# Optimization experiments

Hardware: AMD Instinct MI355X
Metric: run time of the kernel (lower is better)

## Reference

```python
import jax, jax.numpy as jnp
import numpy as np

NEG = jnp.float32(-1e10)

def setup_inputs() -> dict:
    key = jax.random.key(0)
    k1, k2, k3, k4 = jax.random.split(key, 4)
    B, Ns, Nr, D = 64, 512, 256, 1024
    return {
        "span_embeddings": jax.random.normal(k1, (B, Ns, D), dtype=jnp.float32),
        "image_embeddings": jax.random.normal(k2, (B, Nr, D), dtype=jnp.float32),
        "span_mask": jax.random.randint(k3, (B, Ns), 0, 2).astype(jnp.int32),
        "image_mask": jax.random.randint(k4, (B, Nr), 0, 2).astype(jnp.int32),
    }

def reference(span_embeddings, image_embeddings, span_mask, image_mask):
    # pair mask: (B, Ns, Nr) = image_mask[b, None, r] * span_mask[b, s, None]
    mask = (image_mask[:, None, :] * span_mask[:, :, None]).astype(span_embeddings.dtype)
    # QK^T with multiplicative mask, then custom zero->-1e10 masking
    att = jnp.einsum('bsd,brd->bsr', span_embeddings, image_embeddings) * mask
    att = jnp.where(att != 0, att, NEG)
    # spans attend over ROIs
    w_first = jax.nn.softmax(att, axis=-1) * mask
    att_first = jnp.einsum('bsr,brd->bsd', w_first, image_embeddings)
    score = jnp.mean(jnp.square(span_embeddings - att_first))
    # ROIs attend over spans (score_type='both')
    att_t = jnp.swapaxes(att, 1, 2)            # (B, Nr, Ns)
    w_second = jax.nn.softmax(att_t, axis=-1) * jnp.swapaxes(mask, 1, 2)
    att_second = jnp.einsum('brs,bsd->brd', w_second, span_embeddings)
    score = score + jnp.mean(jnp.square(image_embeddings - att_second))
    return score, att_first, att
```

## Files before the change

### kernel.cpp

```cpp
#include <hip/hip_runtime.h>
#include <hip/hip_bf16.h>
#include <math.h>

#define B_  64
#define NS  512
#define NR  256
#define DD  1024
#define NEGV (-1e10f)

typedef __attribute__((ext_vector_type(4))) float f32x4;
typedef __attribute__((ext_vector_type(8))) short bf16x8;

__device__ __forceinline__ unsigned short f2bf(float x) {
    unsigned u = __builtin_bit_cast(unsigned, x);
    unsigned r = u + 0x7FFFu + ((u >> 16) & 1u);
    return (unsigned short)(r >> 16);
}
__device__ __forceinline__ unsigned pk2(float x, float y) {
    unsigned r;
    asm("v_cvt_pk_bf16_f32 %0, %1, %2" : "=v"(r) : "v"(x), "v"(y));
    return r;
}
__device__ __forceinline__ void gload16(const void* g, void* l) {
    __builtin_amdgcn_global_load_lds((const __attribute__((address_space(1))) void*)g,
                                     (__attribute__((address_space(3))) void*)l, 16, 0, 0);
}

__global__ __launch_bounds__(64) void zero_ws(double* ws) {
    if (threadIdx.x == 0) { ws[0] = 0.0; ws[1] = 0.0; }
}

__global__ __launch_bounds__(512) void att_mfma(
    const float* __restrict__ span, const float* __restrict__ image,
    const int* __restrict__ smask, const int* __restrict__ imask,
    float* __restrict__ att, float2* __restrict__ rowP, float2* __restrict__ colP,
    int doStats) {
    const int b  = blockIdx.z;
    const int s0 = blockIdx.y * 128;
    const int r0 = blockIdx.x * 128;
    __shared__ unsigned short Abuf[128][40], Bbuf[128][40];
    const int tid  = threadIdx.x;
    const int lane = tid & 63;
    const int w    = tid >> 6;
    const int wso  = (w >> 2) * 64;
    const int wro  = (w & 3) * 32;
    const float* Sp = span  + ((size_t)b * NS + s0) * DD;
    const float* Im = image + ((size_t)b * NR + r0) * DD;

    f32x4 acc[4][2];
    #pragma unroll
    for (int i = 0; i < 4; ++i)
        #pragma unroll
        for (int j = 0; j < 2; ++j) acc[i][j] = (f32x4){0.f, 0.f, 0.f, 0.f};

    const int row0 = tid >> 2;
    const int kq   = (tid & 3) * 8;
    const int fr   = lane & 15;
    const int fq   = lane >> 4;
    const int fk   = fq * 8;

    for (int k0 = 0; k0 < DD; k0 += 32) {
        {
            const float4 a0 = *reinterpret_cast<const float4*>(Sp + (size_t)row0 * DD + k0 + kq);
            const float4 a1 = *reinterpret_cast<const float4*>(Sp + (size_t)row0 * DD + k0 + kq + 4);
            const float4 c0 = *reinterpret_cast<const float4*>(Im + (size_t)row0 * DD + k0 + kq);
            const float4 c1 = *reinterpret_cast<const float4*>(Im + (size_t)row0 * DD + k0 + kq + 4);
            uint4 u;
            u.x = pk2(a0.x, a0.y); u.y = pk2(a0.z, a0.w);
            u.z = pk2(a1.x, a1.y); u.w = pk2(a1.z, a1.w);
            *reinterpret_cast<uint4*>(&Abuf[row0][kq]) = u;
            u.x = pk2(c0.x, c0.y); u.y = pk2(c0.z, c0.w);
            u.z = pk2(c1.x, c1.y); u.w = pk2(c1.z, c1.w);
            *reinterpret_cast<uint4*>(&Bbuf[row0][kq]) = u;
        }
        __syncthreads();
        bf16x8 ah[4], bh[2];
        #pragma unroll
        for (int mf = 0; mf < 4; ++mf)
            ah[mf] = *reinterpret_cast<const bf16x8*>(&Abuf[wso + mf * 16 + fr][fk]);
        #pragma unroll
        for (int nf = 0; nf < 2; ++nf)
            bh[nf] = *reinterpret_cast<const bf16x8*>(&Bbuf[wro + nf * 16 + fr][fk]);
        #pragma unroll
        for (int mf = 0; mf < 4; ++mf)
            #pragma unroll
            for (int nf = 0; nf < 2; ++nf)
                acc[mf][nf] = __builtin_amdgcn_mfma_f32_16x16x32_bf16(ah[mf], bh[nf], acc[mf][nf], 0, 0, 0);
        __syncthreads();
    }

    float2* rowLDS = reinterpret_cast<float2*>(&Abuf[0][0]);
    float2* colLDS = rowLDS + 512;
    int imv[2];
    #pragma unroll
    for (int nf = 0; nf < 2; ++nf) imv[nf] = imask[b * NR + r0 + wro + nf * 16 + fr];
    float cmax[2] = {-3.4e38f, -3.4e38f};
    float smv[4][4];
    #pragma unroll
    for (int mf = 0; mf < 4; ++mf) {
        #pragma unroll
        for (int i = 0; i < 4; ++i) {
            const int s = s0 + wso + mf * 16 + fq * 4 + i;
            const int sm = smask[b * NS + s];
            smv[mf][i] = (float)sm;
            float* orow = att + ((size_t)b * NS + s) * NR + r0 + wro;
            float vj[2];
            #pragma unroll
            for (int nf = 0; nf < 2; ++nf) {
                float v = acc[mf][nf][i] * (float)(sm * imv[nf]);
                v = (v != 0.0f) ? v : NEGV;
                orow[nf * 16 + fr] = v;
                vj[nf] = v;
                cmax[nf] = fmaxf(cmax[nf], v);
            }
            if (doStats) {
                float rm = fmaxf(vj[0], vj[1]);
                rm = fmaxf(rm, __shfl_xor(rm, 1));
                rm = fmaxf(rm, __shfl_xor(rm, 2));
                rm = fmaxf(rm, __shfl_xor(rm, 4));
                rm = fmaxf(rm, __shfl_xor(rm, 8));
                float rs = __expf(vj[0] - rm) + __expf(vj[1] - rm);
                rs += __shfl_xor(rs, 1);
                rs += __shfl_xor(rs, 2);
                rs += __shfl_xor(rs, 4);
                rs += __shfl_xor(rs, 8);
                if (fr == 0) rowLDS[(wso + mf * 16 + fq * 4 + i) * 4 + (w & 3)] = make_float2(rm, rs);
            }
        }
    }
    if (doStats) {
        #pragma unroll
        for (int nf = 0; nf < 2; ++nf) {
            cmax[nf] = fmaxf(cmax[nf], __shfl_xor(cmax[nf], 16));
            cmax[nf] = fmaxf(cmax[nf], __shfl_xor(cmax[nf], 32));
        }
        float csum[2] = {0.f, 0.f};
        #pragma unroll
        for (int mf = 0; mf < 4; ++mf)
            #pragma unroll
            for (int i = 0; i < 4; ++i)
                #pragma unroll
                for (int nf = 0; nf < 2; ++nf) {
                    float v = acc[mf][nf][i] * (smv[mf][i] * (float)imv[nf]);
                    v = (v != 0.0f) ? v : NEGV;
                    csum[nf] += __expf(v - cmax[nf]);
                }
        #pragma unroll
        for (int nf = 0; nf < 2; ++nf) {
            csum[nf] += __shfl_xor(csum[nf], 16);
            csum[nf] += __shfl_xor(csum[nf], 32);
        }
        if (lane < 16) {
            #pragma unroll
            for (int nf = 0; nf < 2; ++nf)
                colLDS[(wro + nf * 16 + lane) * 2 + (w >> 2)] = make_float2(cmax[nf], csum[nf]);
        }
        __syncthreads();
        if (tid < 128) {
            float2 q0 = rowLDS[tid * 4 + 0], q1 = rowLDS[tid * 4 + 1];
            float2 q2 = rowLDS[tid * 4 + 2], q3 = rowLDS[tid * 4 + 3];
            const float m = fmaxf(fmaxf(q0.x, q1.x), fmaxf(q2.x, q3.x));
            const float ssum = q0.y * __expf(q0.x - m) + q1.y * __expf(q1.x - m)
                             + q2.y * __expf(q2.x - m) + q3.y * __expf(q3.x - m);
            rowP[((size_t)b * NS + s0 + tid) * 2 + blockIdx.x] = make_float2(m, ssum);
        } else if (tid < 256) {
            const int c = tid - 128;
            const float2 q0 = colLDS[c * 2 + 0], q1 = colLDS[c * 2 + 1];
            const float m = fmaxf(q0.x, q1.x);
            const float ssum = q0.y * __expf(q0.x - m) + q1.y * __expf(q1.x - m);
            colP[((size_t)b * NR + r0 + c) * 4 + blockIdx.y] = make_float2(m, ssum);
        }
    }
}

__global__ __launch_bounds__(256) void combine_stats(
    const float2* __restrict__ rowP, const float2* __restrict__ colP,
    const int* __restrict__ smask, const int* __restrict__ imask,
    float* __restrict__ m1, float* __restrict__ f1,
    float* __restrict__ m2, float* __restrict__ f2) {
    const int idx = blockIdx.x * 256 + threadIdx.x;
    if (idx < B_ * NS) {
        const float2 p0 = rowP[(size_t)idx * 2 + 0];
        const float2 p1 = rowP[(size_t)idx * 2 + 1];
        const float m = fmaxf(p0.x, p1.x);
        const float s = p0.y * __expf(p0.x - m) + p1.y * __expf(p1.x - m);
        m1[idx] = m;
        f1[idx] = (float)smask[idx] / s;
    } else if (idx < B_ * NS + B_ * NR) {
        const int j = idx - B_ * NS;
        const float2 p0 = colP[(size_t)j * 4 + 0];
        const float2 p1 = colP[(size_t)j * 4 + 1];
        const float2 p2 = colP[(size_t)j * 4 + 2];
        const float2 p3 = colP[(size_t)j * 4 + 3];
        const float m = fmaxf(fmaxf(p0.x, p1.x), fmaxf(p2.x, p3.x));
        const float s = p0.y * __expf(p0.x - m) + p1.y * __expf(p1.x - m)
                      + p2.y * __expf(p2.x - m) + p3.y * __expf(p3.x - m);
        m2[j] = m;
        f2[j] = (float)imask[j] / s;
    }
}

__global__ __launch_bounds__(256) void transpose_swz(
    const float* __restrict__ src, unsigned short* __restrict__ dst, int N) {
    const int b = blockIdx.z, n0 = blockIdx.y * 32, d0 = blockIdx.x * 32;
    __shared__ unsigned short T[32][36];
    const int t = threadIdx.x;
    {
        const int n = t >> 3, dq = (t & 7) * 4;
        const float4 v = *reinterpret_cast<const float4*>(src + ((size_t)b * N + n0 + n) * DD + d0 + dq);
        T[dq + 0][n] = f2bf(v.x); T[dq + 1][n] = f2bf(v.y);
        T[dq + 2][n] = f2bf(v.z); T[dq + 3][n] = f2bf(v.w);
    }
    __syncthreads();
    {
        const int d = t >> 3, nq = (t & 7) * 4;
        const int dg = d0 + d;
        const int base = n0 + nq;
        const int pos = (base & 63) ^ ((dg & 7) << 3);
        const size_t idx = ((size_t)b * DD + dg) * N + (base & ~63) + pos;
        *reinterpret_cast<ushort4*>(dst + idx) = *reinterpret_cast<const ushort4*>(&T[d][nq]);
    }
}

__global__ __launch_bounds__(256) void build_w12(
    const float* __restrict__ att, const int* __restrict__ smask,
    const int* __restrict__ imask,
    const float* __restrict__ m1, const float* __restrict__ f1,
    const float* __restrict__ m2, const float* __restrict__ f2,
    unsigned short* __restrict__ w1g, unsigned short* __restrict__ w2g) {
    const int b = blockIdx.z, s0 = blockIdx.y * 64, r0 = blockIdx.x * 64;
    __shared__ unsigned short T[64][68];
    __shared__ float m2s[64], f2s[64], ims[64];
    const int tid = threadIdx.x;
    if (tid < 64) {
        m2s[tid] = m2[b * NR + r0 + tid];
        f2s[tid] = f2[b * NR + r0 + tid];
        ims[tid] = (float)imask[b * NR + r0 + tid];
    }
    __syncthreads();
    {
        const int srow = tid >> 2, rg = (tid & 3) * 16;
        const int s = s0 + srow;
        const float m1v = m1[b * NS + s], f1v = f1[b * NS + s];
        const float smv = (float)smask[b * NS + s];
        const float* arow = att + ((size_t)b * NS + s) * NR + r0;
        const int w1swz = (s & 7) << 3;
        unsigned short* w1row = w1g + ((size_t)b * NS + s) * NR + r0;
        #pragma unroll
        for (int g = 0; g < 4; ++g) {
            const int rr = rg + g * 4;
            const float4 a = *reinterpret_cast<const float4*>(arow + rr);
            const float e0 = __expf(a.x - m1v) * f1v * ims[rr + 0];
            const float e1 = __expf(a.y - m1v) * f1v * ims[rr + 1];
            const float e2 = __expf(a.z - m1v) * f1v * ims[rr + 2];
            const float e3 = __expf(a.w - m1v) * f1v * ims[rr + 3];
            uint2 u; u.x = pk2(e0, e1); u.y = pk2(e2, e3);
            *reinterpret_cast<uint2*>(w1row + (rr ^ w1swz)) = u;
            const float q0 = __expf(a.x - m2s[rr + 0]) * f2s[rr + 0] * smv;
            const float q1 = __expf(a.y - m2s[rr + 1]) * f2s[rr + 1] * smv;
            const float q2 = __expf(a.z - m2s[rr + 2]) * f2s[rr + 2] * smv;
            const float q3 = __expf(a.w - m2s[rr + 3]) * f2s[rr + 3] * smv;
            const unsigned t0 = pk2(q0, q1), t1 = pk2(q2, q3);
            T[rr + 0][srow] = (unsigned short)(t0 & 0xFFFF);
            T[rr + 1][srow] = (unsigned short)(t0 >> 16);
            T[rr + 2][srow] = (unsigned short)(t1 & 0xFFFF);
            T[rr + 3][srow] = (unsigned short)(t1 >> 16);
        }
    }
    __syncthreads();
    {
        const int rl = tid >> 2, sg = (tid & 3) * 16;
        const int w2swz = (rl & 7) << 3;
        unsigned short* w2row = w2g + ((size_t)b * NR + r0 + rl) * NS + s0;
        #pragma unroll
        for (int g = 0; g < 4; ++g) {
            const int ss = sg + g * 4;
            *reinterpret_cast<ushort4*>(w2row + (ss ^ w2swz)) =
                *reinterpret_cast<const ushort4*>(&T[rl][ss]);
        }
    }
}

template<int KTOT, int MT, bool WOUT, int WIDX>
__global__ __launch_bounds__(256) void gemm_apply(
    const unsigned short* __restrict__ Ag, const unsigned short* __restrict__ Btg,
    const float* __restrict__ ref, float* __restrict__ outp, double* __restrict__ wsum) {
    const int b = blockIdx.z, m0 = blockIdx.y * 64, d0 = blockIdx.x * 256;
    __shared__ unsigned short As[64 * 64];
    __shared__ unsigned short Bs[256 * 64];
    __shared__ float redsum[256];
    const int tid = threadIdx.x, lane = tid & 63, w = tid >> 6;
    const int fr = lane & 15, fq = lane >> 4;
    f32x4 acc[4][4];
    #pragma unroll
    for (int i = 0; i < 4; ++i)
        #pragma unroll
        for (int j = 0; j < 4; ++j) acc[i][j] = (f32x4){0.f, 0.f, 0.f, 0.f};

    const int srow = tid >> 3;
    const int scol = (tid & 7) * 16;
    for (int kc = 0; kc < KTOT / 64; ++kc) {
        const char* asrc = (const char*)(Ag + ((size_t)b * MT + m0) * KTOT) + kc * 128 + scol;
        #pragma unroll
        for (int c = 0; c < 2; ++c)
            gload16(asrc + (size_t)(c * 32 + srow) * (KTOT * 2), (char*)As + (c * 256 + tid) * 16);
        const char* bsrc = (const char*)(Btg + ((size_t)b * DD + d0) * KTOT) + kc * 128 + scol;
        #pragma unroll
        for (int c = 0; c < 8; ++c)
            gload16(bsrc + (size_t)(c * 32 + srow) * (KTOT * 2), (char*)Bs + (c * 256 + tid) * 16);
        __syncthreads();
        #pragma unroll
        for (int ks = 0; ks < 2; ++ks) {
            bf16x8 aF[4], bF[4];
            #pragma unroll
            for (int mf = 0; mf < 4; ++mf) {
                const int row = mf * 16 + fr;
                const int pos = (ks * 32 + fq * 8) ^ ((row & 7) << 3);
                aF[mf] = *reinterpret_cast<const bf16x8*>(&As[row * 64 + pos]);
            }
            #pragma unroll
            for (int nf = 0; nf < 4; ++nf) {
                const int row = w * 64 + nf * 16 + fr;
                const int pos = (ks * 32 + fq * 8) ^ ((row & 7) << 3);
                bF[nf] = *reinterpret_cast<const bf16x8*>(&Bs[row * 64 + pos]);
            }
            #pragma unroll
            for (int mf = 0; mf < 4; ++mf)
                #pragma unroll
                for (int nf = 0; nf < 4; ++nf)
                    acc[mf][nf] = __builtin_amdgcn_mfma_f32_16x16x32_bf16(aF[mf], bF[nf], acc[mf][nf], 0, 0, 0);
        }
        __syncthreads();
    }
    float sumsq = 0.0f;
    #pragma unroll
    for (int mf = 0; mf < 4; ++mf) {
        #pragma unroll
        for (int i = 0; i < 4; ++i) {
            const int row = m0 + mf * 16 + fq * 4 + i;
            const size_t base = ((size_t)b * MT + row) * DD + d0 + w * 64;
            #pragma unroll
            for (int nf = 0; nf < 4; ++nf) {
                const float v = acc[mf][nf][i];
                const float rv = ref[base + nf * 16 + fr];
                if constexpr (WOUT) outp[base + nf * 16 + fr] = v;
                const float dx = rv - v;
                sumsq += dx * dx;
            }
        }
    }
    redsum[tid] = sumsq; __syncthreads();
    for (int off = 128; off; off >>= 1) {
        if (tid < off) redsum[tid] += redsum[tid + off];
        __syncthreads();
    }
    if (tid == 0) atomicAdd(wsum + WIDX, (double)redsum[0]);
}

__global__ __launch_bounds__(256) void first_kernel(
    const float* __restrict__ span, const float* __restrict__ image,
    const int* __restrict__ smask, const int* __restrict__ imask,
    const float* __restrict__ att, float* __restrict__ att_first,
    double* __restrict__ ws) {
    const int b  = blockIdx.y;
    const int s0 = blockIdx.x * 32;
    __shared__ float wT[256][36];
    __shared__ float Is[32][132];
    __shared__ float red[256];
    const int tid  = threadIdx.x;
    const int lane = tid & 63, wave = tid >> 6;
    for (int i = 0; i < 8; ++i) {
        const int srel = wave * 8 + i;
        const int s    = s0 + srel;
        const float4 v = *reinterpret_cast<const float4*>(att + ((size_t)b * NS + s) * NR + lane * 4);
        float m = fmaxf(fmaxf(v.x, v.y), fmaxf(v.z, v.w));
        #pragma unroll
        for (int off = 32; off; off >>= 1) m = fmaxf(m, __shfl_xor(m, off));
        float4 e;
        e.x = expf(v.x - m); e.y = expf(v.y - m); e.z = expf(v.z - m); e.w = expf(v.w - m);
        float sum = e.x + e.y + e.z + e.w;
        #pragma unroll
        for (int off = 32; off; off >>= 1) sum += __shfl_xor(sum, off);
        const float fac = (float)smask[b * NS + s] / sum;
        const int4 im4 = *reinterpret_cast<const int4*>(imask + b * NR + lane * 4);
        wT[lane * 4 + 0][srel] = e.x * fac * (float)im4.x;
        wT[lane * 4 + 1][srel] = e.y * fac * (float)im4.y;
        wT[lane * 4 + 2][srel] = e.z * fac * (float)im4.z;
        wT[lane * 4 + 3][srel] = e.w * fac * (float)im4.w;
    }
    __syncthreads();
    float sumsq = 0.0f;
    const int txd = tid & 31;
    const int tys = tid >> 5;
    const float* Ib = image + (size_t)b * NR * DD;
    for (int dc = 0; dc < 8; ++dc) {
        const int d0 = dc * 128;
        float acc[4][4] = {};
        for (int rc = 0; rc < 8; ++rc) {
            const int r0 = rc * 32;
            {
                const int rr = tid >> 3;
                const int cb = tid & 7;
                const float* src = Ib + (size_t)(r0 + rr) * DD + d0;
                #pragma unroll
                for (int q = 0; q < 4; ++q)
                    *reinterpret_cast<float4*>(&Is[rr][(cb + 8 * q) * 4]) =
                        *reinterpret_cast<const float4*>(src + (cb + 8 * q) * 4);
            }
            __syncthreads();
            #pragma unroll 4
            for (int rr = 0; rr < 32; ++rr) {
                const float4 wv = *reinterpret_cast<const float4*>(&wT[r0 + rr][tys * 4]);
                const float4 iv = *reinterpret_cast<const float4*>(&Is[rr][txd * 4]);
                const float wvv[4] = {wv.x, wv.y, wv.z, wv.w};
                const float ivv[4] = {iv.x, iv.y, iv.z, iv.w};
                #pragma unroll
                for (int i = 0; i < 4; ++i)
                    #pragma unroll
                    for (int j = 0; j < 4; ++j)
                        acc[i][j] += wvv[i] * ivv[j];
            }
            __syncthreads();
        }
        #pragma unroll
        for (int i = 0; i < 4; ++i) {
            const int s = s0 + tys * 4 + i;
            const size_t base = ((size_t)b * NS + s) * DD + d0 + txd * 4;
            const float4 af = {acc[i][0], acc[i][1], acc[i][2], acc[i][3]};
            *reinterpret_cast<float4*>(att_first + base) = af;
            const float4 sp = *reinterpret_cast<const float4*>(span + base);
            float dx;
            dx = sp.x - af.x; sumsq += dx * dx;
            dx = sp.y - af.y; sumsq += dx * dx;
            dx = sp.z - af.z; sumsq += dx * dx;
            dx = sp.w - af.w; sumsq += dx * dx;
        }
    }
    red[tid] = sumsq; __syncthreads();
    for (int off = 128; off; off >>= 1) {
        if (tid < off) red[tid] += red[tid + off];
        __syncthreads();
    }
    if (tid == 0) atomicAdd(ws, (double)red[0]);
}

__global__ __launch_bounds__(256) void second_kernel(
    const float* __restrict__ span, const float* __restrict__ image,
    const int* __restrict__ smask, const int* __restrict__ imask,
    const float* __restrict__ att, double* __restrict__ ws) {
    const int b  = blockIdx.y;
    const int r0 = blockIdx.x * 32;
    __shared__ float w2s[32][36];
    __shared__ float Ss[32][132];
    __shared__ float mArr[32], fArr[32];
    __shared__ float redm[8][32];
    __shared__ float red[256];
    const int tid = threadIdx.x;
    const int rr = tid & 31, q = tid >> 5;
    const float* attb = att + (size_t)b * NS * NR + r0 + rr;
    float mloc = -3.4e38f;
    for (int t = 0; t < 64; ++t)
        mloc = fmaxf(mloc, attb[(size_t)(q * 64 + t) * NR]);
    redm[q][rr] = mloc;
    __syncthreads();
    if (tid < 32) {
        float m = redm[0][tid];
        #pragma unroll
        for (int qq = 1; qq < 8; ++qq) m = fmaxf(m, redm[qq][tid]);
        mArr[tid] = m;
    }
    __syncthreads();
    const float mcol = mArr[rr];
    float sloc = 0.0f;
    for (int t = 0; t < 64; ++t)
        sloc += expf(attb[(size_t)(q * 64 + t) * NR] - mcol);
    redm[q][rr] = sloc;
    __syncthreads();
    if (tid < 32) {
        float s = 0.0f;
        #pragma unroll
        for (int qq = 0; qq < 8; ++qq) s += redm[qq][tid];
        fArr[tid] = (float)imask[b * NR + r0 + tid] / s;
    }
    __syncthreads();
    float sumsq = 0.0f;
    const int txd = tid & 31;
    const int tyr = tid >> 5;
    const float* Sb = span + (size_t)b * NS * DD;
    for (int dc = 0; dc < 8; ++dc) {
        const int d0 = dc * 128;
        float acc[4][4] = {};
        for (int sc = 0; sc < 16; ++sc) {
            const int sb0 = sc * 32;
            {
                const int sr = tid >> 3;
                const int cb = tid & 7;
                const float* src = Sb + (size_t)(sb0 + sr) * DD + d0;
                #pragma unroll
                for (int qq = 0; qq < 4; ++qq)
                    *reinterpret_cast<float4*>(&Ss[sr][(cb + 8 * qq) * 4]) =
                        *reinterpret_cast<const float4*>(src + (cb + 8 * qq) * 4);
            }
            {
                const int ss = tid >> 3;
                const int rq = (tid & 7) * 4;
                const int s  = sb0 + ss;
                const float4 v = *reinterpret_cast<const float4*>(att + ((size_t)b * NS + s) * NR + r0 + rq);
                const float smv = (float)smask[b * NS + s];
                float4 wv;
                wv.x = expf(v.x - mArr[rq + 0]) * fArr[rq + 0] * smv;
                wv.y = expf(v.y - mArr[rq + 1]) * fArr[rq + 1] * smv;
                wv.z = expf(v.z - mArr[rq + 2]) * fArr[rq + 2] * smv;
                wv.w = expf(v.w - mArr[rq + 3]) * fArr[rq + 3] * smv;
                *reinterpret_cast<float4*>(&w2s[ss][rq]) = wv;
            }
            __syncthreads();
            #pragma unroll 4
            for (int ss = 0; ss < 32; ++ss) {
                const float4 wv = *reinterpret_cast<const float4*>(&w2s[ss][tyr * 4]);
                const float4 sv = *reinterpret_cast<const float4*>(&Ss[ss][txd * 4]);
                const float wvv[4] = {wv.x, wv.y, wv.z, wv.w};
                const float svv[4] = {sv.x, sv.y, sv.z, sv.w};
                #pragma unroll
                for (int i = 0; i < 4; ++i)
                    #pragma unroll
                    for (int j = 0; j < 4; ++j)
                        acc[i][j] += wvv[i] * svv[j];
            }
            __syncthreads();
        }
        #pragma unroll
        for (int i = 0; i < 4; ++i) {
            const int r = r0 + tyr * 4 + i;
            const float4 iv = *reinterpret_cast<const float4*>(image + ((size_t)b * NR + r) * DD + d0 + txd * 4);
            float dx;
            dx = iv.x - acc[i][0]; sumsq += dx * dx;
            dx = iv.y - acc[i][1]; sumsq += dx * dx;
            dx = iv.z - acc[i][2]; sumsq += dx * dx;
            dx = iv.w - acc[i][3]; sumsq += dx * dx;
        }
    }
    red[tid] = sumsq; __syncthreads();
    for (int off = 128; off; off >>= 1) {
        if (tid < off) red[tid] += red[tid + off];
        __syncthreads();
    }
    if (tid == 0) atomicAdd(ws + 1, (double)red[0]);
}

__global__ __launch_bounds__(64) void score_kernel(const double* __restrict__ ws, float* __restrict__ out) {
    if (threadIdx.x == 0) {
        out[0] = (float)(ws[0] / (double)((size_t)B_ * NS * DD) +
                         ws[1] / (double)((size_t)B_ * NR * DD));
    }
}

extern "C" void kernel_launch(void* const* d_in, const int* in_sizes, int n_in,
                              void* d_out, int out_size, void* d_ws, size_t ws_size,
                              hipStream_t stream) {
    const float* span  = (const float*)d_in[0];
    const float* image = (const float*)d_in[1];
    const int*   smask = (const int*)d_in[2];
    const int*   imask = (const int*)d_in[3];
    float* out       = (float*)d_out;
    float* att_first = out + 1;
    float* att       = out + 1 + (size_t)B_ * NS * DD;

    char* base = (char*)d_ws;
    double* wsum = (double*)base;
    float* m1 = (float*)(base + 512);
    float* f1 = m1 + (size_t)B_ * NS;
    float* m2 = f1 + (size_t)B_ * NS;
    float* f2 = m2 + (size_t)B_ * NR;
    float2* rowP = (float2*)(f2 + (size_t)B_ * NR);
    float2* colP = rowP + (size_t)B_ * NS * 2;
    char* X0 = (char*)(colP + (size_t)B_ * NR * 4);
    unsigned short* imgT = (unsigned short*)X0;
    unsigned short* w1g  = (unsigned short*)(X0 + (size_t)B_ * DD * NR * 2);
    unsigned short* spT  = (unsigned short*)X0;
    unsigned short* w2g  = (unsigned short*)(X0 + (size_t)B_ * DD * NS * 2);
    const size_t NEED = (size_t)(X0 - base) + (size_t)B_ * DD * NS * 2 + (size_t)B_ * NS * NR * 2;
    const int wsok = (ws_size >= NEED) ? 1 : 0;

    zero_ws<<<dim3(1), dim3(64), 0, stream>>>(wsum);
    att_mfma<<<dim3(NR / 128, NS / 128, B_), dim3(512), 0, stream>>>(
        span, image, smask, imask, att, rowP, colP, wsok);

    if (wsok) {
        combine_stats<<<dim3((B_ * NS + B_ * NR) / 256), dim3(256), 0, stream>>>(
            rowP, colP, smask, imask, m1, f1, m2, f2);
        transpose_swz<<<dim3(DD / 32, NR / 32, B_), dim3(256), 0, stream>>>(image, imgT, NR);
        build_w12<<<dim3(NR / 64, NS / 64, B_), dim3(256), 0, stream>>>(
            att, smask, imask, m1, f1, m2, f2, w1g, w2g);
        gemm_apply<NR, NS, true, 0><<<dim3(DD / 256, NS / 64, B_), dim3(256), 0, stream>>>(
            w1g, imgT, span, att_first, wsum);
        transpose_swz<<<dim3(DD / 32, NS / 32, B_), dim3(256), 0, stream>>>(span, spT, NS);
        gemm_apply<NS, NR, false, 1><<<dim3(DD / 256, NR / 64, B_), dim3(256), 0, stream>>>(
            w2g, spT, image, nullptr, wsum);
    } else {
        first_kernel<<<dim3(NS / 32, B_), dim3(256), 0, stream>>>(span, image, smask, imask, att, att_first, wsum);
        second_kernel<<<dim3(NR / 32, B_), dim3(256), 0, stream>>>(span, image, smask, imask, att, wsum);
    }
    score_kernel<<<dim3(1), dim3(64), 0, stream>>>(wsum, out);
}
```

Baseline: 317.1 us.

## Double-buffer LDS with register prefetch in att_mfma and remap block order by batch

The QK^T GEMM loop now keeps two LDS buffers and loads the next k-slice of fp32 data into registers while MFMAs run on the current buffer, which cuts the synchronisation stalls per iteration. The grid is flattened to 1D with batch as the fastest-varying index, changing which blocks run concurrently and how tiles are spread across CUs and cache. This doubles the LDS footprint and raises register use for the prefetched float4s, which may lower occupancy.

```diff
diff --git a/kernel.cpp b/kernel.cpp
--- a/kernel.cpp
+++ b/kernel.cpp
@@ -35,10 +35,13 @@
     const int* __restrict__ smask, const int* __restrict__ imask,
     float* __restrict__ att, float2* __restrict__ rowP, float2* __restrict__ colP,
     int doStats) {
-    const int b  = blockIdx.z;
-    const int s0 = blockIdx.y * 128;
-    const int r0 = blockIdx.x * 128;
-    __shared__ unsigned short Abuf[128][40], Bbuf[128][40];
+    const int id = blockIdx.x;
+    const int b  = id & 63;
+    const int ys = (id >> 6) & 3;
+    const int xr = id >> 8;
+    const int s0 = ys * 128;
+    const int r0 = xr * 128;
+    __shared__ unsigned short Abuf[2][128][40], Bbuf[2][128][40];
     const int tid  = threadIdx.x;
     const int lane = tid & 63;
     const int w    = tid >> 6;
@@ -59,37 +62,54 @@
     const int fq   = lane >> 4;
     const int fk   = fq * 8;
 
-    for (int k0 = 0; k0 < DD; k0 += 32) {
-        {
-            const float4 a0 = *reinterpret_cast<const float4*>(Sp + (size_t)row0 * DD + k0 + kq);
-            const float4 a1 = *reinterpret_cast<const float4*>(Sp + (size_t)row0 * DD + k0 + kq + 4);
-            const float4 c0 = *reinterpret_cast<const float4*>(Im + (size_t)row0 * DD + k0 + kq);
-            const float4 c1 = *reinterpret_cast<const float4*>(Im + (size_t)row0 * DD + k0 + kq + 4);
-            uint4 u;
-            u.x = pk2(a0.x, a0.y); u.y = pk2(a0.z, a0.w);
-            u.z = pk2(a1.x, a1.y); u.w = pk2(a1.z, a1.w);
-            *reinterpret_cast<uint4*>(&Abuf[row0][kq]) = u;
-            u.x = pk2(c0.x, c0.y); u.y = pk2(c0.z, c0.w);
-            u.z = pk2(c1.x, c1.y); u.w = pk2(c1.z, c1.w);
-            *reinterpret_cast<uint4*>(&Bbuf[row0][kq]) = u;
-        }
-        __syncthreads();
+    float4 ra[4], rb[4];
+    auto LOADR = [&](float4* r, int k0) {
+        r[0] = *reinterpret_cast<const float4*>(Sp + (size_t)row0 * DD + k0 + kq);
+        r[1] = *reinterpret_cast<const float4*>(Sp + (size_t)row0 * DD + k0 + kq + 4);
+        r[2] = *reinterpret_cast<const float4*>(Im + (size_t)row0 * DD + k0 + kq);
+        r[3] = *reinterpret_cast<const float4*>(Im + (size_t)row0 * DD + k0 + kq + 4);
+    };
+    auto CVTW = [&](const float4* r, int buf) {
+        uint4 u;
+        u.x = pk2(r[0].x, r[0].y); u.y = pk2(r[0].z, r[0].w);
+        u.z = pk2(r[1].x, r[1].y); u.w = pk2(r[1].z, r[1].w);
+        *reinterpret_cast<uint4*>(&Abuf[buf][row0][kq]) = u;
+        u.x = pk2(r[2].x, r[2].y); u.y = pk2(r[2].z, r[2].w);
+        u.z = pk2(r[3].x, r[3].y); u.w = pk2(r[3].z, r[3].w);
+        *reinterpret_cast<uint4*>(&Bbuf[buf][row0][kq]) = u;
+    };
+    auto MFMAS = [&](int buf) {
         bf16x8 ah[4], bh[2];
         #pragma unroll
         for (int mf = 0; mf < 4; ++mf)
-            ah[mf] = *reinterpret_cast<const bf16x8*>(&Abuf[wso + mf * 16 + fr][fk]);
+            ah[mf] = *reinterpret_cast<const bf16x8*>(&Abuf[buf][wso + mf * 16 + fr][fk]);
         #pragma unroll
         for (int nf = 0; nf < 2; ++nf)
-            bh[nf] = *reinterpret_cast<const bf16x8*>(&Bbuf[wro + nf * 16 + fr][fk]);
+            bh[nf] = *reinterpret_cast<const bf16x8*>(&Bbuf[buf][wro + nf * 16 + fr][fk]);
         #pragma unroll
         for (int mf = 0; mf < 4; ++mf)
             #pragma unroll
             for (int nf = 0; nf < 2; ++nf)
                 acc[mf][nf] = __builtin_amdgcn_mfma_f32_16x16x32_bf16(ah[mf], bh[nf], acc[mf][nf], 0, 0, 0);
-        __syncthreads();
-    }
-
-    float2* rowLDS = reinterpret_cast<float2*>(&Abuf[0][0]);
+    };
+
+    LOADR(ra, 0);
+    CVTW(ra, 0);
+    LOADR(rb, 32);
+    __syncthreads();
+    for (int kk = 0; kk < 16; ++kk) {
+        const int k = kk * 2;
+        if (k + 2 < 32) LOADR(ra, (k + 2) * 32);
+        MFMAS(0);
+        CVTW(rb, 1);
+        __syncthreads();
+        if (k + 3 < 32) LOADR(rb, (k + 3) * 32);
+        MFMAS(1);
+        if (k + 2 < 32) CVTW(ra, 0);
+        __syncthreads();
+    }
+
+    float2* rowLDS = reinterpret_cast<float2*>(&Abuf[0][0][0]);
     float2* colLDS = rowLDS + 512;
     int imv[2];
     #pragma unroll
@@ -162,13 +182,13 @@
             const float m = fmaxf(fmaxf(q0.x, q1.x), fmaxf(q2.x, q3.x));
             const float ssum = q0.y * __expf(q0.x - m) + q1.y * __expf(q1.x - m)
                              + q2.y * __expf(q2.x - m) + q3.y * __expf(q3.x - m);
-            rowP[((size_t)b * NS + s0 + tid) * 2 + blockIdx.x] = make_float2(m, ssum);
+            rowP[((size_t)b * NS + s0 + tid) * 2 + xr] = make_float2(m, ssum);
         } else if (tid < 256) {
             const int c = tid - 128;
             const float2 q0 = colLDS[c * 2 + 0], q1 = colLDS[c * 2 + 1];
             const float m = fmaxf(q0.x, q1.x);
             const float ssum = q0.y * __expf(q0.x - m) + q1.y * __expf(q1.x - m);
-            colP[((size_t)b * NR + r0 + c) * 4 + blockIdx.y] = make_float2(m, ssum);
+            colP[((size_t)b * NR + r0 + c) * 4 + ys] = make_float2(m, ssum);
         }
     }
 }
@@ -583,7 +603,7 @@
     const int wsok = (ws_size >= NEED) ? 1 : 0;
 
     zero_ws<<<dim3(1), dim3(64), 0, stream>>>(wsum);
-    att_mfma<<<dim3(NR / 128, NS / 128, B_), dim3(512), 0, stream>>>(
+    att_mfma<<<dim3(512), dim3(512), 0, stream>>>(
         span, image, smask, imask, att, rowP, colP, wsok);
 
     if (wsok) {
```

Result: faster. 287.5 us (-9.3%).
